# Kernel tuning notes

Measured on AMD Instinct MI355X. Metric: run time of the kernel, lower is better.

## Reference

```python
import jax, jax.numpy as jnp
import numpy as np

EPS = 1e-5  # clamp floor on learnable input scale (elastic quantizer)


def setup_inputs() -> dict:
    key = jax.random.key(0)
    k0, k1, k2, k3 = jax.random.split(key, 4)
    B, S, H = 8, 4096, 1024
    hidden_states = jax.random.normal(k0, (B, S, H), dtype=jnp.float32)
    W = jax.random.normal(k1, (H, H), dtype=jnp.float32) * 0.02
    b = jax.random.normal(k2, (H,), dtype=jnp.float32) * 0.02
    alpha = jax.random.uniform(k3, (1,), dtype=jnp.float32) + 0.1  # learnable input scale
    return {"hidden_states": hidden_states, "W": W, "b": b, "alpha": alpha}


def reference(hidden_states, W, b, alpha):
    # index_select first token along dim=-2 -> [B, 1, H]
    first_token = hidden_states[..., 0:1, :]
    # elastic 1-bit signed input quantization: x_q = sign(x) * alpha (alpha clamped)
    a = jnp.maximum(alpha, EPS)
    x_q = jnp.sign(first_token) * a
    # BWN weight quantization (layerwise): w_q = sign(W) * mean(|W|)
    w_scale = jnp.mean(jnp.abs(W))
    w_q = jnp.sign(W) * w_scale
    # linear: y = x_q @ w_q^T + b, then tanh
    out = jnp.einsum('bsh,oh->bso', x_q, w_q) + b
    return jnp.tanh(out)
```

## Files before the change

### kernel.cpp

```cpp
#include <hip/hip_runtime.h>
#include <hip/hip_bf16.h>
#include <math.h>

#define HDIM 1024
#define BATCH 8
#define SEQ 4096

#define U64_WSGN 0
#define U64_WNZ  (16 * 1024)
#define U64_XSGN (32 * 1024)
#define U64_XNZ  (32 * 1024 + 128)
#define U64_TOT  (32 * 1024 + 256)

__global__ __launch_bounds__(256) void k_masks(const float* __restrict__ hs,
                                               const float* __restrict__ W,
                                               unsigned long long* __restrict__ ws64,
                                               float* __restrict__ wabs) {
    const int tid = threadIdx.x;
    const int wave = tid >> 6, lane = tid & 63;

    const bool isW = blockIdx.x < 256;
    int o = 0, b = 0;
    const float* row;
    if (isW) { o = blockIdx.x * 4 + wave; row = W + (size_t)o * HDIM; }
    else     { b = (blockIdx.x - 256) * 4 + wave; row = hs + (size_t)b * SEQ * HDIM; }

    float aabs = 0.f;
    #pragma unroll
    for (int k = 0; k < 4; ++k) {
        float4 v = *reinterpret_cast<const float4*>(row + k * 256 + lane * 4);
        float e0 = v.x, e1 = v.y, e2 = v.z, e3 = v.w;
        const float ee[4] = {e0, e1, e2, e3};
        #pragma unroll
        for (int j = 0; j < 4; ++j) {
            unsigned long long sg = __ballot(ee[j] < 0.f);
            unsigned long long nz = __ballot(ee[j] != 0.f);
            const int w = k * 4 + j;
            if (lane == 0) {
                if (isW) {
                    ws64[U64_WSGN + w * 1024 + o] = sg;
                    ws64[U64_WNZ  + w * 1024 + o] = nz;
                } else {
                    ws64[U64_XSGN + b * 16 + w] = sg;
                    ws64[U64_XNZ  + b * 16 + w] = nz;
                }
            }
            aabs += fabsf(ee[j]);
        }
    }
    if (isW) {
        #pragma unroll
        for (int off = 32; off >= 1; off >>= 1) aabs += __shfl_down(aabs, off, 64);
        if (lane == 0) wabs[o] = aabs;
    }
}

__global__ __launch_bounds__(256) void k_out(const unsigned long long* __restrict__ ws64,
                                             const float* __restrict__ wabs,
                                             const float* __restrict__ bias,
                                             const float* __restrict__ alpha,
                                             float* __restrict__ out) {
    __shared__ float red[256];
    __shared__ unsigned long long lx[32];
    const int tid = threadIdx.x;
    const int b = blockIdx.x >> 2;
    const int o = (blockIdx.x & 3) * 256 + tid;

    if (tid < 16)       lx[tid] = ws64[U64_XSGN + b * 16 + tid];
    else if (tid < 32)  lx[tid] = ws64[U64_XNZ + b * 16 + (tid - 16)];

    red[tid] = wabs[tid] + wabs[tid + 256] + wabs[tid + 512] + wabs[tid + 768];
    __syncthreads();
    #pragma unroll
    for (int off = 128; off >= 1; off >>= 1) {
        if (tid < off) red[tid] += red[tid + off];
        __syncthreads();
    }

    int n = 0, d = 0;
    #pragma unroll
    for (int w = 0; w < 16; ++w) {
        unsigned long long wsg = ws64[U64_WSGN + w * 1024 + o];
        unsigned long long wnz = ws64[U64_WNZ  + w * 1024 + o];
        unsigned long long u = wnz & lx[16 + w];
        unsigned long long m = (wsg ^ lx[w]) & u;
        n += __popcll(u);
        d += __popcll(m);
    }

    float a = alpha[0];
    if (a < 1e-5f) a = 1e-5f;
    const float scale = a * red[0] * (1.0f / 1048576.0f);
    out[b * HDIM + o] = tanhf(scale * (float)(n - 2 * d) + bias[o]);
}

extern "C" void kernel_launch(void* const* d_in, const int* in_sizes, int n_in,
                              void* d_out, int out_size, void* d_ws, size_t ws_size,
                              hipStream_t stream) {
    const float* hs    = (const float*)d_in[0];
    const float* W     = (const float*)d_in[1];
    const float* bias  = (const float*)d_in[2];
    const float* alpha = (const float*)d_in[3];
    float* out = (float*)d_out;

    unsigned long long* ws64 = (unsigned long long*)d_ws;
    float* wabs = (float*)(ws64 + U64_TOT);

    k_masks<<<258, 256, 0, stream>>>(hs, W, ws64, wabs);
    k_out<<<(BATCH * HDIM) / 256, 256, 0, stream>>>(ws64, wabs, bias, alpha, out);
}
```

Measured before the change: 13.49 us.

## Fuse mask and output kernels into one cooperative kernel with grid sync

Merges the two launches into a single cooperative kernel of 256 blocks. Each wave packs one W row into sign and nonzero bitmasks; waves 0-7 also pack one batch's first token. A grid-wide sync then separates this from the popcount dot-product stage. That stage is remapped so each wave handles one output across all 8 batches, with 8 lanes per batch reduced by shuffles, and the weight-abs partials are pre-reduced per block. The aim is to remove the second launch overhead and the inter-kernel gap, at the cost of a cooperative launch and a grid barrier.

```diff
diff --git a/kernel.cpp b/kernel.cpp
--- a/kernel.cpp
+++ b/kernel.cpp
@@ -1,6 +1,8 @@
 #include <hip/hip_runtime.h>
-#include <hip/hip_bf16.h>
+#include <hip/hip_cooperative_groups.h>
 #include <math.h>
+
+namespace cg = cooperative_groups;
 
 #define HDIM 1024
 #define BATCH 8
@@ -12,86 +14,107 @@
 #define U64_XNZ  (32 * 1024 + 128)
 #define U64_TOT  (32 * 1024 + 256)
 
-__global__ __launch_bounds__(256) void k_masks(const float* __restrict__ hs,
+__global__ __launch_bounds__(256) void k_fused(const float* __restrict__ hs,
                                                const float* __restrict__ W,
+                                               const float* __restrict__ bias,
+                                               const float* __restrict__ alpha,
+                                               float* __restrict__ out,
                                                unsigned long long* __restrict__ ws64,
-                                               float* __restrict__ wabs) {
+                                               float* __restrict__ wpart) {
+    __shared__ float swabs[4];
+    __shared__ float red[256];
+    __shared__ unsigned long long lxs[128];
+    __shared__ unsigned long long lxn[128];
+
     const int tid = threadIdx.x;
     const int wave = tid >> 6, lane = tid & 63;
+    const int g = blockIdx.x * 4 + wave;
 
-    const bool isW = blockIdx.x < 256;
-    int o = 0, b = 0;
-    const float* row;
-    if (isW) { o = blockIdx.x * 4 + wave; row = W + (size_t)o * HDIM; }
-    else     { b = (blockIdx.x - 256) * 4 + wave; row = hs + (size_t)b * SEQ * HDIM; }
+    {
+        const float* row = W + (size_t)g * HDIM;
+        float aabs = 0.f;
+        #pragma unroll
+        for (int k = 0; k < 4; ++k) {
+            float4 v = *reinterpret_cast<const float4*>(row + k * 256 + lane * 4);
+            const float ee[4] = {v.x, v.y, v.z, v.w};
+            #pragma unroll
+            for (int j = 0; j < 4; ++j) {
+                unsigned long long sg = __ballot(ee[j] < 0.f);
+                unsigned long long nz = __ballot(ee[j] != 0.f);
+                const int w = k * 4 + j;
+                if (lane == 0) {
+                    ws64[U64_WSGN + w * 1024 + g] = sg;
+                    ws64[U64_WNZ  + w * 1024 + g] = nz;
+                }
+                aabs += fabsf(ee[j]);
+            }
+        }
+        #pragma unroll
+        for (int off = 32; off >= 1; off >>= 1) aabs += __shfl_down(aabs, off, 64);
+        if (lane == 0) swabs[wave] = aabs;
 
-    float aabs = 0.f;
-    #pragma unroll
-    for (int k = 0; k < 4; ++k) {
-        float4 v = *reinterpret_cast<const float4*>(row + k * 256 + lane * 4);
-        float e0 = v.x, e1 = v.y, e2 = v.z, e3 = v.w;
-        const float ee[4] = {e0, e1, e2, e3};
-        #pragma unroll
-        for (int j = 0; j < 4; ++j) {
-            unsigned long long sg = __ballot(ee[j] < 0.f);
-            unsigned long long nz = __ballot(ee[j] != 0.f);
-            const int w = k * 4 + j;
-            if (lane == 0) {
-                if (isW) {
-                    ws64[U64_WSGN + w * 1024 + o] = sg;
-                    ws64[U64_WNZ  + w * 1024 + o] = nz;
-                } else {
-                    ws64[U64_XSGN + b * 16 + w] = sg;
-                    ws64[U64_XNZ  + b * 16 + w] = nz;
+        if (g < BATCH) {
+            const float* xr = hs + (size_t)g * SEQ * HDIM;
+            #pragma unroll
+            for (int k = 0; k < 4; ++k) {
+                float4 v = *reinterpret_cast<const float4*>(xr + k * 256 + lane * 4);
+                const float ee[4] = {v.x, v.y, v.z, v.w};
+                #pragma unroll
+                for (int j = 0; j < 4; ++j) {
+                    unsigned long long sg = __ballot(ee[j] < 0.f);
+                    unsigned long long nz = __ballot(ee[j] != 0.f);
+                    const int w = k * 4 + j;
+                    if (lane == 0) {
+                        ws64[U64_XSGN + g * 16 + w] = sg;
+                        ws64[U64_XNZ  + g * 16 + w] = nz;
+                    }
                 }
             }
-            aabs += fabsf(ee[j]);
         }
     }
-    if (isW) {
-        #pragma unroll
-        for (int off = 32; off >= 1; off >>= 1) aabs += __shfl_down(aabs, off, 64);
-        if (lane == 0) wabs[o] = aabs;
-    }
-}
+    __syncthreads();
+    if (tid == 0) wpart[blockIdx.x] = swabs[0] + swabs[1] + swabs[2] + swabs[3];
 
-__global__ __launch_bounds__(256) void k_out(const unsigned long long* __restrict__ ws64,
-                                             const float* __restrict__ wabs,
-                                             const float* __restrict__ bias,
-                                             const float* __restrict__ alpha,
-                                             float* __restrict__ out) {
-    __shared__ float red[256];
-    __shared__ unsigned long long lx[32];
-    const int tid = threadIdx.x;
-    const int b = blockIdx.x >> 2;
-    const int o = (blockIdx.x & 3) * 256 + tid;
+    cg::this_grid().sync();
 
-    if (tid < 16)       lx[tid] = ws64[U64_XSGN + b * 16 + tid];
-    else if (tid < 32)  lx[tid] = ws64[U64_XNZ + b * 16 + (tid - 16)];
-
-    red[tid] = wabs[tid] + wabs[tid + 256] + wabs[tid + 512] + wabs[tid + 768];
+    if (tid < 128)      lxs[tid] = ws64[U64_XSGN + tid];
+    else                lxn[tid - 128] = ws64[U64_XNZ + (tid - 128)];
+    red[tid] = wpart[tid];
     __syncthreads();
     #pragma unroll
     for (int off = 128; off >= 1; off >>= 1) {
         if (tid < off) red[tid] += red[tid + off];
         __syncthreads();
     }
-
-    int n = 0, d = 0;
-    #pragma unroll
-    for (int w = 0; w < 16; ++w) {
-        unsigned long long wsg = ws64[U64_WSGN + w * 1024 + o];
-        unsigned long long wnz = ws64[U64_WNZ  + w * 1024 + o];
-        unsigned long long u = wnz & lx[16 + w];
-        unsigned long long m = (wsg ^ lx[w]) & u;
-        n += __popcll(u);
-        d += __popcll(m);
-    }
-
     float a = alpha[0];
     if (a < 1e-5f) a = 1e-5f;
     const float scale = a * red[0] * (1.0f / 1048576.0f);
-    out[b * HDIM + o] = tanhf(scale * (float)(n - 2 * d) + bias[o]);
+
+    const int o = g;
+    const int b = lane >> 3;
+    const int sub = lane & 7;
+    const int w0 = 2 * sub, w1 = 2 * sub + 1;
+
+    unsigned long long wsg0 = ws64[U64_WSGN + w0 * 1024 + o];
+    unsigned long long wnz0 = ws64[U64_WNZ  + w0 * 1024 + o];
+    unsigned long long wsg1 = ws64[U64_WSGN + w1 * 1024 + o];
+    unsigned long long wnz1 = ws64[U64_WNZ  + w1 * 1024 + o];
+
+    unsigned long long u0 = wnz0 & lxn[b * 16 + w0];
+    unsigned long long m0 = (wsg0 ^ lxs[b * 16 + w0]) & u0;
+    unsigned long long u1 = wnz1 & lxn[b * 16 + w1];
+    unsigned long long m1 = (wsg1 ^ lxs[b * 16 + w1]) & u1;
+
+    int n = __popcll(u0) + __popcll(u1);
+    int d = __popcll(m0) + __popcll(m1);
+    #pragma unroll
+    for (int s = 1; s < 8; s <<= 1) {
+        n += __shfl_xor(n, s, 8);
+        d += __shfl_xor(d, s, 8);
+    }
+    if (sub == 0) {
+        out[b * HDIM + o] = tanhf(scale * (float)(n - 2 * d) + bias[o]);
+    }
 }
 
 extern "C" void kernel_launch(void* const* d_in, const int* in_sizes, int n_in,
@@ -104,8 +127,10 @@
     float* out = (float*)d_out;
 
     unsigned long long* ws64 = (unsigned long long*)d_ws;
-    float* wabs = (float*)(ws64 + U64_TOT);
+    float* wpart = (float*)(ws64 + U64_TOT);
 
-    k_masks<<<258, 256, 0, stream>>>(hs, W, ws64, wabs);
-    k_out<<<(BATCH * HDIM) / 256, 256, 0, stream>>>(ws64, wabs, bias, alpha, out);
+    void* args[] = {(void*)&hs, (void*)&W, (void*)&bias, (void*)&alpha,
+                    (void*)&out, (void*)&ws64, (void*)&wpart};
+    hipLaunchCooperativeKernel(reinterpret_cast<void*>(k_fused),
+                               dim3(256), dim3(256), args, 0, stream);
 }
```

After: 47.92 us. 255% more time.
